# Performance work log

Measured on AMD Instinct MI355X. Metric: run time of the kernel, lower is better.

Reference implementation:

```python
import jax, jax.numpy as jnp
import numpy as np
from jax import lax

B, N, CIN, COUT, NPOINT, K = 8, 4096, 64, 128, 1024, 24
EPS = 1e-5


def setup_inputs() -> dict:
    key = jax.random.key(0)
    ks = jax.random.split(key, 16)
    def conv_w(k, o, i):
        return jax.random.normal(k, (o, i), jnp.float32) * (1.0 / np.sqrt(i))
    inp = {
        "xyz": jax.random.normal(ks[0], (B, N, 3), jnp.float32),
        "x": jax.random.normal(ks[1], (B, CIN, N), jnp.float32),
        "farthest0": jax.random.randint(ks[2], (B,), 0, N),
        # Local.proj: Conv1DBR (CIN -> COUT, k=1, no bias)
        "W_proj": conv_w(ks[3], COUT, CIN), "g_proj": jnp.ones(COUT), "b_proj": jnp.zeros(COUT),
        # Local.channel: one Conv1DBRRes (COUT -> COUT -> COUT)
        "W_la1": conv_w(ks[4], COUT, COUT), "g_la1": jnp.ones(COUT), "b_la1": jnp.zeros(COUT),
        "W_la2": conv_w(ks[5], COUT, COUT), "g_la2": jnp.ones(COUT), "b_la2": jnp.zeros(COUT),
        # ca: one Conv1DBRRes (COUT -> COUT -> COUT)
        "W_ca1": conv_w(ks[6], COUT, COUT), "g_ca1": jnp.ones(COUT), "b_ca1": jnp.zeros(COUT),
        "W_ca2": conv_w(ks[7], COUT, COUT), "g_ca2": jnp.ones(COUT), "b_ca2": jnp.zeros(COUT),
    }
    return inp


def _bn(z, g, b):
    # BatchNorm1d in training mode: biased batch stats over (batch, length)
    mu = z.mean((0, 2), keepdims=True)
    var = z.var((0, 2), keepdims=True)
    return g[None, :, None] * (z - mu) * lax.rsqrt(var + EPS) + b[None, :, None]


def _conv(z, W):  # kernel_size=1 Conv1d == channel matmul
    return jnp.einsum('oc,mcl->mol', W, z)


def _resblock(z, W1, g1, b1, W2, g2, b2):
    y = jax.nn.relu(_bn(_conv(z, W1), g1, b1))
    y = _bn(_conv(y, W2), g2, b2)
    return jax.nn.relu(y + z)


def _forward(xyz, x, farthest0,
             W_proj, g_proj, b_proj,
             W_la1, g_la1, b_la1, W_la2, g_la2, b_la2,
             W_ca1, g_ca1, b_ca1, W_ca2, g_ca2, b_ca2):
    Bv, Nv, _ = xyz.shape
    xt = jnp.transpose(x, (0, 2, 1))  # [B, N, C]

    # --- farthest point sampling (sequential, vectorized over batch) ---
    def step(carry, _):
        dist, far = carry
        c = jnp.take_along_axis(xyz, far[:, None, None], axis=1)  # [B,1,3]
        d = jnp.sum((xyz - c) ** 2, -1)                           # [B,N]
        dist = jnp.minimum(dist, d)
        return (dist, jnp.argmax(dist, -1)), far

    init = (jnp.full((Bv, Nv), 1e10, xyz.dtype), farthest0)
    _, cent = lax.scan(step, init, None, length=NPOINT)
    fps_idx = cent.T  # [B, NPOINT]

    new_xyz = jnp.take_along_axis(xyz, fps_idx[:, :, None], axis=1)  # [B,NP,3]
    new_pts = jnp.take_along_axis(xt, fps_idx[:, :, None], axis=1)   # [B,NP,C]

    # --- kNN grouping: squared distances [B, NP, N], smallest-K indices ---
    d2 = (jnp.sum(new_xyz ** 2, -1)[:, :, None]
          + jnp.sum(xyz ** 2, -1)[:, None, :]
          - 2.0 * jnp.einsum('bpc,bnc->bpn', new_xyz, xyz))
    _, knn = lax.top_k(-d2, K)  # [B, NP, K]
    grouped = jax.vmap(lambda p, i: p[i])(xt, knn)  # [B, NP, K, C]
    edge = grouped - new_pts[:, :, None, :]         # [B, NP, K, C]

    # --- Local: per-group conv-BN-ReLU + residual block + max over K ---
    M = Bv * NPOINT
    h = jnp.transpose(edge, (0, 1, 3, 2)).reshape(M, edge.shape[-1], K)  # [M, CIN, K]
    h = jax.nn.relu(_bn(_conv(h, W_proj), g_proj, b_proj))
    h = _resblock(h, W_la1, g_la1, b_la1, W_la2, g_la2, b_la2)
    h = h.max(-1)  # adaptive_max_pool1d(.,1) -> [M, COUT]
    h = h.reshape(Bv, NPOINT, -1).transpose(0, 2, 1)  # [B, COUT, NP]

    # --- Channel (ca) ---
    h = _resblock(h, W_ca1, g_ca1, b_ca1, W_ca2, g_ca2, b_ca2)
    return new_xyz, h


def reference(xyz, x, farthest0,
              W_proj, g_proj, b_proj,
              W_la1, g_la1, b_la1, W_la2, g_la2, b_la2,
              W_ca1, g_ca1, b_ca1, W_ca2, g_ca2, b_ca2):
    return _forward(xyz, x, farthest0,
                    W_proj, g_proj, b_proj,
                    W_la1, g_la1, b_la1, W_la2, g_la2, b_la2,
                    W_ca1, g_ca1, b_ca1, W_ca2, g_ca2, b_ca2)
```

## Files before the change

### kernel.cpp

```cpp
#include <hip/hip_runtime.h>

#define BB 8
#define NN 4096
#define CIN 64
#define COUTC 128
#define NPT 1024
#define KNN 24

typedef unsigned short u16;
typedef unsigned int u32;
typedef unsigned long long u64;

using short8v = __attribute__((ext_vector_type(8))) short;
using f32x4  = __attribute__((ext_vector_type(4))) float;
using f32x2  = __attribute__((ext_vector_type(2))) float;

__device__ __forceinline__ u16 f2bf(float f){ u32 u=__float_as_uint(f); u += 0x7FFFu + ((u>>16)&1u); return (u16)(u>>16); }
__device__ __forceinline__ float bf2f(u16 h){ return __uint_as_float(((u32)h)<<16); }

template<int C> __device__ __forceinline__ float dppmax_f32(float x){
  int y=__builtin_amdgcn_update_dpp(__float_as_int(x),__float_as_int(x),C,0xF,0xF,false);
  return fmaxf(x,__int_as_float(y));
}
template<int C> __device__ __forceinline__ u32 dppmin_u32(u32 x){
  u32 y=(u32)__builtin_amdgcn_update_dpp((int)x,(int)x,C,0xF,0xF,false);
  return y<x?y:x;
}
template<int C> __device__ __forceinline__ void dppmax_u64p(u32& lo, u32& hi){
  u32 nlo=(u32)__builtin_amdgcn_update_dpp((int)lo,(int)lo,C,0xF,0xF,false);
  u32 nhi=(u32)__builtin_amdgcn_update_dpp((int)hi,(int)hi,C,0xF,0xF,false);
  bool g=(nhi>hi)||((nhi==hi)&&(nlo>lo));
  lo=g?nlo:lo; hi=g?nhi:hi;
}
__device__ __forceinline__ f32x2 vmin2(f32x2 a, f32x2 b){
#if __has_builtin(__builtin_elementwise_min)
  return __builtin_elementwise_min(a,b);
#else
  f32x2 r; r.x=fminf(a.x,b.x); r.y=fminf(a.y,b.y); return r;
#endif
}
__device__ __forceinline__ f32x2 vmax2(f32x2 a, f32x2 b){
#if __has_builtin(__builtin_elementwise_max)
  return __builtin_elementwise_max(a,b);
#else
  f32x2 r; r.x=fmaxf(a.x,b.x); r.y=fmaxf(a.y,b.y); return r;
#endif
}

__global__ __launch_bounds__(256) void xt_kern(const float* __restrict__ x, float* __restrict__ xt){
  __shared__ float tile[64][68];
  int blk=blockIdx.x; int b=blk>>6; int n0=(blk&63)<<6;
  int t=threadIdx.x;
  {
    int c=t>>2, nj=(t&3)*16;
    const float4* gp=reinterpret_cast<const float4*>(x + ((size_t)(b*64+c))*NN + n0+nj);
    #pragma unroll
    for(int j=0;j<4;j++){
      float4 v=gp[j];
      *reinterpret_cast<float4*>(&tile[c][nj+4*j])=v;
    }
  }
  __syncthreads();
  {
    int n=t>>2, c16=(t&3)*16;
    size_t base=((size_t)(b*NN+n0+n))*64 + c16;
    #pragma unroll
    for(int j=0;j<4;j++){
      *reinterpret_cast<float4*>(xt+base+4*j)=
        make_float4(tile[c16+4*j][n],tile[c16+4*j+1][n],tile[c16+4*j+2][n],tile[c16+4*j+3][n]);
    }
  }
}

__global__ __launch_bounds__(256) void sn_kern(const float* __restrict__ xyz, float* __restrict__ sn){
  int i=blockIdx.x*256+threadIdx.x;
  const float* p=xyz+(size_t)i*3;
  float x=p[0], y=p[1], z=p[2];
  sn[i]=__fadd_rn(__fadd_rn(__fmul_rn(x,x),__fmul_rn(y,y)),__fmul_rn(z,z));
}

__global__ __launch_bounds__(256) void fps_kern(const float* __restrict__ xyz,
    const int* __restrict__ far0, int* __restrict__ fps_idx)
{
  __shared__ float4 lp[NN];
  __shared__ u64 mkey[2][4];
  const int b=blockIdx.x, t=threadIdx.x, w=t>>6, l=t&63;
  f32x2 px2[8],py2[8],pz2[8],d2v[8];
  {
    float4 q[12];
    const float4* gp=reinterpret_cast<const float4*>(xyz+(size_t)b*NN*3)+(size_t)t*12;
    #pragma unroll
    for(int i=0;i<12;i++) q[i]=gp[i];
    const float* v=reinterpret_cast<const float*>(q);
    #pragma unroll
    for(int j=0;j<8;j++){
      px2[j]=(f32x2){v[6*j+0],v[6*j+3]};
      py2[j]=(f32x2){v[6*j+1],v[6*j+4]};
      pz2[j]=(f32x2){v[6*j+2],v[6*j+5]};
      lp[t*16+2*j  ]=make_float4(v[6*j+0],v[6*j+1],v[6*j+2],0.f);
      lp[t*16+2*j+1]=make_float4(v[6*j+3],v[6*j+4],v[6*j+5],0.f);
      d2v[j]=(f32x2){1e10f,1e10f};
    }
  }
  __syncthreads();
  int far=far0[b];
  float4 c=lp[far];
  int par=0;
  for(int it=0;it<NPT;++it){
    if(t==0) fps_idx[b*NPT+it]=far;
    f32x2 cx2=(f32x2){c.x,c.x}, cy2=(f32x2){c.y,c.y}, cz2=(f32x2){c.z,c.z};
    f32x2 m2=(f32x2){-1.f,-1.f};
    #pragma unroll
    for(int j=0;j<8;j++){
      f32x2 dx=px2[j]-cx2, dy=py2[j]-cy2, dz=pz2[j]-cz2;
      f32x2 d=(dx*dx+dy*dy)+dz*dz;
      f32x2 nd=vmin2(d2v[j],d); d2v[j]=nd;
      m2=vmax2(m2,nd);
    }
    float m0=fmaxf(m2.x,m2.y);
    if(it==NPT-1) break;
    float r=m0;
    r=dppmax_f32<0x111>(r); r=dppmax_f32<0x112>(r); r=dppmax_f32<0x114>(r);
    r=dppmax_f32<0x118>(r); r=dppmax_f32<0x142>(r); r=dppmax_f32<0x143>(r);
    float wmax=__int_as_float(__builtin_amdgcn_readlane(__float_as_int(r),63));
    u64 bal=__ballot(m0==wmax);
    int winlane=__ffsll((unsigned long long)bal)-1;
    int myj=15;
    #pragma unroll
    for(int j=7;j>=0;--j){
      if(d2v[j].y==m0) myj=2*j+1;
      if(d2v[j].x==m0) myj=2*j;
    }
    int widx_w=__builtin_amdgcn_readlane(t*16+myj,winlane);
    if(l==0) mkey[par][w]=(((u64)__float_as_uint(wmax))<<32)|(u32)(~(u32)widx_w);
    __syncthreads();
    u64 k4=mkey[par][l&3];
    u32 klo=(u32)k4, khi=(u32)(k4>>32);
    dppmax_u64p<0xB1>(klo,khi);
    dppmax_u64p<0x4E>(klo,khi);
    int widx=(int)(~klo);
    far=widx;
    c=lp[widx];
    par^=1;
  }
}

__global__ __launch_bounds__(256) void knn_kern(const float* __restrict__ xyz,
  const float* __restrict__ sn, const int* __restrict__ fps,
  const float* __restrict__ xt, u16* __restrict__ edge, float* __restrict__ outxyz)
{
  __shared__ u64 mkey[2][4];
  __shared__ int sel[KNN];
  const int m=blockIdx.x, b=m>>10;
  const int t=threadIdx.x, w=t>>6, l=t&63;
  const int ctr=fps[m];
  const float sp=sn[b*NN+ctr];
  float cx,cy,cz;
  { const float* cp=xyz+((size_t)b*NN+ctr)*3; cx=cp[0]; cy=cp[1]; cz=cp[2]; }
  u32 key[16];
  {
    float4 q[12];
    const float4* gp=reinterpret_cast<const float4*>(xyz+((size_t)b*NN)*3+(size_t)t*48);
    #pragma unroll
    for(int i=0;i<12;i++) q[i]=gp[i];
    const float* v=reinterpret_cast<const float*>(q);
    float snl[16];
    const float4* sp4=reinterpret_cast<const float4*>(sn+b*NN+t*16);
    #pragma unroll
    for(int i=0;i<4;i++){ float4 s4=sp4[i]; snl[4*i]=s4.x; snl[4*i+1]=s4.y; snl[4*i+2]=s4.z; snl[4*i+3]=s4.w; }
    #pragma unroll
    for(int j=0;j<16;j++){
      float nx=v[3*j], ny=v[3*j+1], nz=v[3*j+2];
      float dot=__fadd_rn(__fadd_rn(__fmul_rn(cx,nx),__fmul_rn(cy,ny)),__fmul_rn(cz,nz));
      float d2=__fsub_rn(__fadd_rn(sp,snl[j]),__fmul_rn(2.f,dot));
      u32 bbv=__float_as_uint(d2);
      key[j]=(bbv&0x80000000u)?~bbv:(bbv|0x80000000u);
    }
  }
  u32 loc=0xFFFFFFFFu; int myj=0;
  #pragma unroll
  for(int j=15;j>=0;--j){ if(key[j]<=loc){ loc=key[j]; myj=j; } }
  int par=0;
  for(int rd=0;rd<KNN;rd++){
    u32 r=loc;
    r=dppmin_u32<0x111>(r); r=dppmin_u32<0x112>(r); r=dppmin_u32<0x114>(r);
    r=dppmin_u32<0x118>(r); r=dppmin_u32<0x142>(r); r=dppmin_u32<0x143>(r);
    u32 wmin=(u32)__builtin_amdgcn_readlane((int)r,63);
    u64 bal=__ballot(loc==wmin);
    int winlane=__ffsll((unsigned long long)bal)-1;
    int widx_w=__builtin_amdgcn_readlane(t*16+myj,winlane);
    if(l==0) mkey[par][w]=(((u64)wmin)<<32)|(u32)widx_w;
    __syncthreads();
    u64 b0=mkey[par][0],b1=mkey[par][1],b2=mkey[par][2],b3=mkey[par][3];
    u64 bb0=b0<b1?b0:b1, bb1=b2<b3?b2:b3, best=bb0<bb1?bb0:bb1;
    int widx=(int)(u32)(best&0xFFFFFFFFull);
    if(t==(widx>>4)){
      key[widx&15]=0xFFFFFFFFu;
      loc=0xFFFFFFFFu; myj=0;
      #pragma unroll
      for(int j=15;j>=0;--j){ if(key[j]<=loc){ loc=key[j]; myj=j; } }
    }
    if(t==0) sel[rd]=widx;
    par^=1;
  }
  if(t<3) outxyz[(size_t)m*3+t]=xyz[((size_t)b*NN+ctr)*3+t];
  __syncthreads();
  {
    int r=t>>3, c0=(t&7)*8;
    if(r<KNN){
      int nb=sel[r];
      const float* np_=xt+((size_t)b*NN+nb)*64+c0;
      const float* cp_=xt+((size_t)b*NN+ctr)*64+c0;
      float4 n0=*reinterpret_cast<const float4*>(np_);
      float4 n1=*reinterpret_cast<const float4*>(np_+4);
      float4 c0v=*reinterpret_cast<const float4*>(cp_);
      float4 c1v=*reinterpret_cast<const float4*>(cp_+4);
      u32 ov[4];
      ov[0]=(u32)f2bf(__fsub_rn(n0.x,c0v.x))|((u32)f2bf(__fsub_rn(n0.y,c0v.y))<<16);
      ov[1]=(u32)f2bf(__fsub_rn(n0.z,c0v.z))|((u32)f2bf(__fsub_rn(n0.w,c0v.w))<<16);
      ov[2]=(u32)f2bf(__fsub_rn(n1.x,c1v.x))|((u32)f2bf(__fsub_rn(n1.y,c1v.y))<<16);
      ov[3]=(u32)f2bf(__fsub_rn(n1.z,c1v.z))|((u32)f2bf(__fsub_rn(n1.w,c1v.w))<<16);
      *reinterpret_cast<uint4*>(edge+((size_t)m*KNN+r)*64+c0)=make_uint4(ov[0],ov[1],ov[2],ov[3]);
    }
  }
}

template<int KD, bool XF>
__global__ __launch_bounds__(256) void gemm_bn(
    const u16* __restrict__ A, const float* __restrict__ W,
    const float* __restrict__ af, const float* __restrict__ cf,
    u16* __restrict__ Z, float* __restrict__ pSum, float* __restrict__ pSq,
    int nblk4)
{
  extern __shared__ char smem[];
  u16* lA=(u16*)smem;
  u16* lW=lA+128*KD;
  const int t=threadIdx.x, blk=blockIdx.x;
  constexpr int TPR=KD/8;
  constexpr int RPP=256/TPR;
  constexpr int NPASS=128/RPP;
  const int rl=t/TPR, c0=(t%TPR)*8;
  float ax[8], cxx[8];
  if constexpr (XF){
    #pragma unroll
    for(int j=0;j<8;j++){ ax[j]=af[c0+j]; cxx[j]=cf[c0+j]; }
  }
  #pragma unroll
  for(int p=0;p<NPASS;p++){
    int row=p*RPP+rl;
    uint4 v=*reinterpret_cast<const uint4*>(A+((size_t)blk*128+row)*KD+c0);
    if constexpr (XF){
      u32 in[4]={v.x,v.y,v.z,v.w}; u32 out[4];
      #pragma unroll
      for(int q2=0;q2<4;q2++){
        float f0=__uint_as_float((in[q2]&0xFFFFu)<<16);
        float f1=__uint_as_float(in[q2]&0xFFFF0000u);
        f0=fmaxf(fmaf(ax[2*q2],f0,cxx[2*q2]),0.f);
        f1=fmaxf(fmaf(ax[2*q2+1],f1,cxx[2*q2+1]),0.f);
        out[q2]=(u32)f2bf(f0)|((u32)f2bf(f1)<<16);
      }
      v.x=out[0]; v.y=out[1]; v.z=out[2]; v.w=out[3];
    }
    int byte=row*(KD*2)+c0*2; byte^=(row&7)<<4;
    *reinterpret_cast<uint4*>((char*)lA+byte)=v;
    const float* wp_=W+(size_t)row*KD+c0;
    float4 w0=*reinterpret_cast<const float4*>(wp_);
    float4 w1=*reinterpret_cast<const float4*>(wp_+4);
    uint4 wv;
    wv.x=(u32)f2bf(w0.x)|((u32)f2bf(w0.y)<<16);
    wv.y=(u32)f2bf(w0.z)|((u32)f2bf(w0.w)<<16);
    wv.z=(u32)f2bf(w1.x)|((u32)f2bf(w1.y)<<16);
    wv.w=(u32)f2bf(w1.z)|((u32)f2bf(w1.w)<<16);
    int wbyte=row*(KD*2)+c0*2; wbyte^=(row&7)<<4;
    *reinterpret_cast<uint4*>((char*)lW+wbyte)=wv;
  }
  __syncthreads();
  const int l=t&63, w2=t>>6;
  const int l15=l&15, qq=l>>4;
  f32x4 acc[2][8];
  #pragma unroll
  for(int r=0;r<2;r++)
    #pragma unroll
    for(int f=0;f<8;f++) acc[r][f]=(f32x4){0.f,0.f,0.f,0.f};
  #pragma unroll
  for(int s=0;s<KD/32;s++){
    short8v a[2];
    #pragma unroll
    for(int r=0;r<2;r++){
      int row=w2*32+r*16+l15;
      int byte=row*(KD*2)+s*64+qq*16; byte^=(row&7)<<4;
      a[r]=*reinterpret_cast<const short8v*>((char*)lA+byte);
    }
    #pragma unroll
    for(int f=0;f<8;f++){
      int row=f*16+l15;
      int byte=row*(KD*2)+s*64+qq*16; byte^=(row&7)<<4;
      short8v bb=*reinterpret_cast<const short8v*>((char*)lW+byte);
      acc[0][f]=__builtin_amdgcn_mfma_f32_16x16x32_bf16(a[0],bb,acc[0][f],0,0,0);
      acc[1][f]=__builtin_amdgcn_mfma_f32_16x16x32_bf16(a[1],bb,acc[1][f],0,0,0);
    }
  }
  #pragma unroll
  for(int f=0;f<8;f++){
    float sv=0.f,qv=0.f;
    #pragma unroll
    for(int r=0;r<2;r++){
      int grow=blk*128+w2*32+r*16+qq*4;
      #pragma unroll
      for(int j=0;j<4;j++){
        float v=acc[r][f][j];
        Z[((size_t)(grow+j))*128+f*16+l15]=f2bf(v);
        sv+=v; qv+=v*v;
      }
    }
    sv+=__shfl_xor(sv,16); sv+=__shfl_xor(sv,32);
    qv+=__shfl_xor(qv,16); qv+=__shfl_xor(qv,32);
    if(l<16){
      int col=f*16+l15;
      pSum[(size_t)col*nblk4+blk*4+w2]=sv;
      pSq [(size_t)col*nblk4+blk*4+w2]=qv;
    }
  }
}

__global__ __launch_bounds__(256) void stats_kern(
  const float* __restrict__ pSum, const float* __restrict__ pSq,
  const float* __restrict__ g, const float* __restrict__ bb,
  float* __restrict__ af, float* __restrict__ cf, int nparts, float inv_cnt)
{
  int ch=blockIdx.x, t=threadIdx.x;
  float s=0.f,q=0.f;
  for(int i=t;i<nparts;i+=256){ s+=pSum[(size_t)ch*nparts+i]; q+=pSq[(size_t)ch*nparts+i]; }
  #pragma unroll
  for(int o=1;o<64;o<<=1){ s+=__shfl_xor(s,o); q+=__shfl_xor(q,o); }
  __shared__ float ls[4], lq[4];
  int w=t>>6, l=t&63;
  if(l==0){ ls[w]=s; lq[w]=q; }
  __syncthreads();
  if(t==0){
    float S=ls[0]+ls[1]+ls[2]+ls[3], Q=lq[0]+lq[1]+lq[2]+lq[3];
    float mu=S*inv_cnt, var=Q*inv_cnt-mu*mu;
    float a=g[ch]/sqrtf(var+1e-5f);
    af[ch]=a; cf[ch]=bb[ch]-mu*a;
  }
}

__global__ __launch_bounds__(256) void pool_kern(const u16* __restrict__ z3, const u16* __restrict__ z1,
  const float* __restrict__ af1, const float* __restrict__ cf1,
  const float* __restrict__ af3, const float* __restrict__ cf3, u16* __restrict__ pooled)
{
  int t=threadIdx.x;
  int g=blockIdx.x*2+(t>>7);
  int c=t&127;
  float a1=af1[c],c1=cf1[c],a3=af3[c],c3=cf3[c];
  float mmax=0.f;
  size_t base=(size_t)g*KNN*128+c;
  #pragma unroll 4
  for(int k=0;k<KNN;k++){
    float v3=bf2f(z3[base+(size_t)k*128]);
    float v1=bf2f(z1[base+(size_t)k*128]);
    float z1p=fmaxf(fmaf(a1,v1,c1),0.f);
    float v=fmaf(a3,v3,c3)+z1p;
    mmax=fmaxf(mmax,fmaxf(v,0.f));
  }
  pooled[(size_t)g*128+c]=f2bf(mmax);
}

__global__ __launch_bounds__(256) void final_kern(const u16* __restrict__ z5,
  const u16* __restrict__ pooled, const float* __restrict__ af, const float* __restrict__ cf,
  float* __restrict__ outh)
{
  __shared__ float tile[64][68];
  int blk=blockIdx.x; int b=blk>>5; int tl=blk&31; int p0=(tl&15)<<6; int o0=(tl>>4)<<6;
  int t=threadIdx.x;
  {
    int pl=t>>2, o1=(t&3)*16;
    size_t base=((size_t)(b*1024+p0+pl))*128 + o0+o1;
    #pragma unroll
    for(int h2=0;h2<2;h2++){
      uint4 v5=*reinterpret_cast<const uint4*>(z5+base+h2*8);
      uint4 vp=*reinterpret_cast<const uint4*>(pooled+base+h2*8);
      u32 a5[4]={v5.x,v5.y,v5.z,v5.w}; u32 pp[4]={vp.x,vp.y,vp.z,vp.w};
      #pragma unroll
      for(int q2=0;q2<4;q2++){
        int oj=o1+h2*8+q2*2;
        float g0=af[o0+oj],h0=cf[o0+oj],g1=af[o0+oj+1],h1=cf[o0+oj+1];
        float f0=__uint_as_float((a5[q2]&0xFFFFu)<<16);
        float f1=__uint_as_float(a5[q2]&0xFFFF0000u);
        float q0=__uint_as_float((pp[q2]&0xFFFFu)<<16);
        float q1=__uint_as_float(pp[q2]&0xFFFF0000u);
        tile[oj][pl]  =fmaxf(fmaf(g0,f0,h0)+q0,0.f);
        tile[oj+1][pl]=fmaxf(fmaf(g1,f1,h1)+q1,0.f);
      }
    }
  }
  __syncthreads();
  {
    int ol=t>>2, pj=(t&3)*16;
    size_t obase=((size_t)(b*128+o0+ol))*1024 + p0+pj;
    #pragma unroll
    for(int j=0;j<4;j++){
      *reinterpret_cast<float4*>(outh+obase+4*j)=
        make_float4(tile[ol][pj+4*j],tile[ol][pj+4*j+1],tile[ol][pj+4*j+2],tile[ol][pj+4*j+3]);
    }
  }
}

extern "C" void kernel_launch(void* const* d_in, const int* in_sizes, int n_in,
                              void* d_out, int out_size, void* d_ws, size_t ws_size,
                              hipStream_t stream)
{
  (void)in_sizes; (void)n_in; (void)out_size; (void)ws_size;
  const float* xyz   =(const float*)d_in[0];
  const float* x     =(const float*)d_in[1];
  const int*   far0  =(const int*)d_in[2];
  const float* W_proj=(const float*)d_in[3];
  const float* g_proj=(const float*)d_in[4];
  const float* b_proj=(const float*)d_in[5];
  const float* W_la1 =(const float*)d_in[6];
  const float* g_la1 =(const float*)d_in[7];
  const float* b_la1 =(const float*)d_in[8];
  const float* W_la2 =(const float*)d_in[9];
  const float* g_la2 =(const float*)d_in[10];
  const float* b_la2 =(const float*)d_in[11];
  const float* W_ca1 =(const float*)d_in[12];
  const float* g_ca1 =(const float*)d_in[13];
  const float* b_ca1 =(const float*)d_in[14];
  const float* W_ca2 =(const float*)d_in[15];
  const float* g_ca2 =(const float*)d_in[16];
  const float* b_ca2 =(const float*)d_in[17];

  char* ws=(char*)d_ws;
  const size_t OFF_XT =0;
  const size_t OFF_SN =8388608;
  const size_t OFF_FPS=8519680;
  const size_t OFF_AF =8552448;
  const size_t OFF_CF =8555008;
  const size_t OFF_PS =8557568;
  const size_t OFF_PQ =11703296;
  const size_t OFF_PL =14849024;
  const size_t OFF_Z4 =16946176;
  const size_t OFF_Z5 =19043328;
  const size_t OFF_Z1 =21140480;
  const size_t OFF_B2 =71472128;

  float* xt  =(float*)(ws+OFF_XT);
  float* sn  =(float*)(ws+OFF_SN);
  int* fps   =(int*)(ws+OFF_FPS);
  float* af  =(float*)(ws+OFF_AF);
  float* cf  =(float*)(ws+OFF_CF);
  float* pS  =(float*)(ws+OFF_PS);
  float* pQ  =(float*)(ws+OFF_PQ);
  u16* pooled=(u16*)(ws+OFF_PL);
  u16* z4    =(u16*)(ws+OFF_Z4);
  u16* z5    =(u16*)(ws+OFF_Z5);
  u16* z1    =(u16*)(ws+OFF_Z1);
  u16* edge  =(u16*)(ws+OFF_B2);
  u16* z2    =(u16*)(ws+OFF_B2);
  u16* z3    =(u16*)(ws+OFF_B2);
  float* outxyz=(float*)d_out;
  float* outh  =(float*)d_out+24576;

  const float invL=1.f/196608.f, invC=1.f/8192.f;

  xt_kern<<<512,256,0,stream>>>(x,xt);
  sn_kern<<<128,256,0,stream>>>(xyz,sn);
  fps_kern<<<8,256,0,stream>>>(xyz,far0,fps);
  knn_kern<<<8192,256,0,stream>>>(xyz,sn,fps,xt,edge,outxyz);

  gemm_bn<64,false><<<1536,256,32768,stream>>>(edge,W_proj,nullptr,nullptr,z1,pS,pQ,6144);
  stats_kern<<<128,256,0,stream>>>(pS,pQ,g_proj,b_proj,af+0,cf+0,6144,invL);

  gemm_bn<128,true><<<1536,256,65536,stream>>>(z1,W_la1,af+0,cf+0,z2,pS,pQ,6144);
  stats_kern<<<128,256,0,stream>>>(pS,pQ,g_la1,b_la1,af+128,cf+128,6144,invL);

  gemm_bn<128,true><<<1536,256,65536,stream>>>(z2,W_la2,af+128,cf+128,z3,pS,pQ,6144);
  stats_kern<<<128,256,0,stream>>>(pS,pQ,g_la2,b_la2,af+256,cf+256,6144,invL);

  pool_kern<<<4096,256,0,stream>>>(z3,z1,af+0,cf+0,af+256,cf+256,pooled);

  gemm_bn<128,false><<<64,256,65536,stream>>>(pooled,W_ca1,nullptr,nullptr,z4,pS,pQ,256);
  stats_kern<<<128,256,0,stream>>>(pS,pQ,g_ca1,b_ca1,af+384,cf+384,256,invC);

  gemm_bn<128,true><<<64,256,65536,stream>>>(z4,W_ca2,af+384,cf+384,z5,pS,pQ,256);
  stats_kern<<<128,256,0,stream>>>(pS,pQ,g_ca2,b_ca2,af+512,cf+512,256,invC);

  final_kern<<<256,256,0,stream>>>(z5,pooled,af+512,cf+512,outh);
}
```

Baseline: 830.8 us.

## Pack two batches per FPS block using half-wavefronts

The farthest-point-sampling kernel now handles two batches per 256-thread block. Each 32-lane half of a wavefront serves one batch, and each thread holds 32 points instead of 16. The wave reductions stop at 32 lanes, and the cross-wave argmax is done with eight shared keys, read per half. This halves the FPS grid and shortens the DPP reduction chain, but doubles the per-thread distance work in every sequential iteration and doubles shared memory use.

After: 1.220 ms. 46.9% more time.

```diff
diff --git a/kernel.cpp b/kernel.cpp
--- a/kernel.cpp
+++ b/kernel.cpp
@@ -82,65 +82,82 @@
 __global__ __launch_bounds__(256) void fps_kern(const float* __restrict__ xyz,
     const int* __restrict__ far0, int* __restrict__ fps_idx)
 {
-  __shared__ float4 lp[NN];
-  __shared__ u64 mkey[2][4];
-  const int b=blockIdx.x, t=threadIdx.x, w=t>>6, l=t&63;
-  f32x2 px2[8],py2[8],pz2[8],d2v[8];
-  {
-    float4 q[12];
-    const float4* gp=reinterpret_cast<const float4*>(xyz+(size_t)b*NN*3)+(size_t)t*12;
-    #pragma unroll
-    for(int i=0;i<12;i++) q[i]=gp[i];
-    const float* v=reinterpret_cast<const float*>(q);
-    #pragma unroll
-    for(int j=0;j<8;j++){
-      px2[j]=(f32x2){v[6*j+0],v[6*j+3]};
-      py2[j]=(f32x2){v[6*j+1],v[6*j+4]};
-      pz2[j]=(f32x2){v[6*j+2],v[6*j+5]};
-      lp[t*16+2*j  ]=make_float4(v[6*j+0],v[6*j+1],v[6*j+2],0.f);
-      lp[t*16+2*j+1]=make_float4(v[6*j+3],v[6*j+4],v[6*j+5],0.f);
-      d2v[j]=(f32x2){1e10f,1e10f};
+  __shared__ float4 lp[2][NN];
+  __shared__ u64 mkey[2][8];
+  const int t=threadIdx.x, w=t>>6, l=t&63;
+  const int half=l>>5, lh=l&31;
+  const int b=blockIdx.x*2+half;
+  const int pbase=w*1024+lh*32;
+  f32x2 px2[16],py2[16],pz2[16],d2v[16];
+  {
+    const float4* gp=reinterpret_cast<const float4*>(xyz+((size_t)b*NN+pbase)*3);
+    #pragma unroll
+    for(int h2=0;h2<2;h2++){
+      float4 q[12];
+      #pragma unroll
+      for(int i=0;i<12;i++) q[i]=gp[h2*12+i];
+      const float* v=reinterpret_cast<const float*>(q);
+      #pragma unroll
+      for(int j=0;j<8;j++){
+        int jj=h2*8+j;
+        px2[jj]=(f32x2){v[6*j+0],v[6*j+3]};
+        py2[jj]=(f32x2){v[6*j+1],v[6*j+4]};
+        pz2[jj]=(f32x2){v[6*j+2],v[6*j+5]};
+        lp[half][pbase+2*jj  ]=make_float4(v[6*j+0],v[6*j+1],v[6*j+2],0.f);
+        lp[half][pbase+2*jj+1]=make_float4(v[6*j+3],v[6*j+4],v[6*j+5],0.f);
+        d2v[jj]=(f32x2){1e10f,1e10f};
+      }
     }
   }
   __syncthreads();
   int far=far0[b];
-  float4 c=lp[far];
+  float4 c=lp[half][far];
   int par=0;
   for(int it=0;it<NPT;++it){
-    if(t==0) fps_idx[b*NPT+it]=far;
+    if(w==0&&lh==0) fps_idx[b*NPT+it]=far;
     f32x2 cx2=(f32x2){c.x,c.x}, cy2=(f32x2){c.y,c.y}, cz2=(f32x2){c.z,c.z};
-    f32x2 m2=(f32x2){-1.f,-1.f};
-    #pragma unroll
-    for(int j=0;j<8;j++){
+    #pragma unroll
+    for(int j=0;j<16;j++){
       f32x2 dx=px2[j]-cx2, dy=py2[j]-cy2, dz=pz2[j]-cz2;
       f32x2 d=(dx*dx+dy*dy)+dz*dz;
-      f32x2 nd=vmin2(d2v[j],d); d2v[j]=nd;
-      m2=vmax2(m2,nd);
-    }
+      d2v[j]=vmin2(d2v[j],d);
+    }
+    f32x2 m2=d2v[0];
+    #pragma unroll
+    for(int j=1;j<16;j++) m2=vmax2(m2,d2v[j]);
     float m0=fmaxf(m2.x,m2.y);
     if(it==NPT-1) break;
     float r=m0;
     r=dppmax_f32<0x111>(r); r=dppmax_f32<0x112>(r); r=dppmax_f32<0x114>(r);
-    r=dppmax_f32<0x118>(r); r=dppmax_f32<0x142>(r); r=dppmax_f32<0x143>(r);
-    float wmax=__int_as_float(__builtin_amdgcn_readlane(__float_as_int(r),63));
-    u64 bal=__ballot(m0==wmax);
-    int winlane=__ffsll((unsigned long long)bal)-1;
-    int myj=15;
-    #pragma unroll
-    for(int j=7;j>=0;--j){
+    r=dppmax_f32<0x118>(r); r=dppmax_f32<0x142>(r);
+    float wmaxA=__int_as_float(__builtin_amdgcn_readlane(__float_as_int(r),31));
+    float wmaxB=__int_as_float(__builtin_amdgcn_readlane(__float_as_int(r),63));
+    float wv=half?wmaxB:wmaxA;
+    u64 bal=__ballot(m0==wv);
+    int winA=(int)__ffsll((unsigned long long)(bal&0xFFFFFFFFull))-1;
+    int winB=32+(int)__ffsll((unsigned long long)(bal>>32))-1;
+    int myj=31;
+    #pragma unroll
+    for(int j=15;j>=0;--j){
       if(d2v[j].y==m0) myj=2*j+1;
       if(d2v[j].x==m0) myj=2*j;
     }
-    int widx_w=__builtin_amdgcn_readlane(t*16+myj,winlane);
-    if(l==0) mkey[par][w]=(((u64)__float_as_uint(wmax))<<32)|(u32)(~(u32)widx_w);
+    int gidx=pbase+myj;
+    int widxA=__builtin_amdgcn_readlane(gidx,winA);
+    int widxB=__builtin_amdgcn_readlane(gidx,winB);
+    if(l==0)  mkey[par][w]  =(((u64)__float_as_uint(wmaxA))<<32)|(u32)(~(u32)((widxA<<2)|w));
+    if(l==32) mkey[par][4+w]=(((u64)__float_as_uint(wmaxB))<<32)|(u32)(~(u32)((widxB<<2)|w));
     __syncthreads();
-    u64 k4=mkey[par][l&3];
-    u32 klo=(u32)k4, khi=(u32)(k4>>32);
+    u64 k=mkey[par][l&7];
+    u32 klo=(u32)k, khi=(u32)(k>>32);
     dppmax_u64p<0xB1>(klo,khi);
     dppmax_u64p<0x4E>(klo,khi);
-    int widx=(int)(~klo);
-    far=widx;
-    c=lp[widx];
+    u32 loA=(u32)__builtin_amdgcn_readlane((int)klo,0);
+    u32 loB=(u32)__builtin_amdgcn_readlane((int)klo,4);
+    int farA=(int)((~loA)>>2)&4095;
+    int farB=(int)((~loB)>>2)&4095;
+    far=half?farB:farA;
+    c=lp[half][far];
     par^=1;
   }
 }
@@ -465,7 +482,7 @@
 
   xt_kern<<<512,256,0,stream>>>(x,xt);
   sn_kern<<<128,256,0,stream>>>(xyz,sn);
-  fps_kern<<<8,256,0,stream>>>(xyz,far0,fps);
+  fps_kern<<<4,256,0,stream>>>(xyz,far0,fps);
   knn_kern<<<8192,256,0,stream>>>(xyz,sn,fps,xt,edge,outxyz);
 
   gemm_bn<64,false><<<1536,256,32768,stream>>>(edge,W_proj,nullptr,nullptr,z1,pS,pQ,6144);
```
